# Kernel optimization log

Hardware: AMD Instinct MI355X
Metric: run time of the kernel (lower is better)

Reference implementation:

```python
import jax, jax.numpy as jnp
import numpy as np

POOL = 7          # pool_size (hardcoded 7x7 bins in source)
TOTAL_BINS = POOL * POOL  # 49
ALPHA = 32        # channels per position-sensitive group
NUM_ROIS = 8192
H = W = 20        # feature-map size; source hardcodes img_w=img_h=20 for normalization
CROP = 2          # bin_crop_size = 14 // 7


def setup_inputs() -> dict:
    key = jax.random.key(0)
    k1, k2, k3 = jax.random.split(key, 3)
    img = jax.random.normal(k1, (1, H, W, TOTAL_BINS * ALPHA), dtype=jnp.float32)
    xy = jax.random.uniform(k2, (1, NUM_ROIS, 2), minval=0.0, maxval=14.0, dtype=jnp.float32)
    wh = jax.random.uniform(k3, (1, NUM_ROIS, 2), minval=2.0, maxval=6.0, dtype=jnp.float32)
    rois = jnp.concatenate([xy, wh], axis=-1)  # (1, R, 4) as (x, y, w, h)
    return {"img": img, "rois": rois}


def _ps_roi_align(img, rois):
    R = rois.shape[1]
    x, y, w, h = rois[0, :, 0], rois[0, :, 1], rois[0, :, 2], rois[0, :, 3]
    step_y = h / POOL
    step_x = w / POOL

    # bin index b = bin_x * POOL + bin_y (outer loop bin_x, inner bin_y in source)
    bin_x = jnp.repeat(jnp.arange(POOL, dtype=jnp.float32), POOL)  # (49,)
    bin_y = jnp.tile(jnp.arange(POOL, dtype=jnp.float32), POOL)    # (49,)

    # normalized box coords [y1, x1, y2, x2] per (bin, roi)
    y1 = (y[None, :] + bin_y[:, None] * step_y[None, :]) / 20.0          # (49, R)
    x1 = (x[None, :] + bin_x[:, None] * step_x[None, :]) / 20.0
    y2 = (y[None, :] + (bin_y[:, None] + 1.0) * step_y[None, :]) / 20.0
    x2 = (x[None, :] + (bin_x[:, None] + 1.0) * step_x[None, :]) / 20.0

    # tf.image.crop_and_resize with crop size (2,2): sample points are exactly
    # the box corners in pixel space: y1*(H-1), y2*(H-1) (and same for x).
    ys = jnp.stack([y1, y2], axis=-1) * (H - 1)  # (49, R, 2)
    xs = jnp.stack([x1, x2], axis=-1) * (W - 1)  # (49, R, 2)

    valid_y = (ys >= 0) & (ys <= H - 1)  # (49, R, 2)
    valid_x = (xs >= 0) & (xs <= W - 1)

    fy = jnp.floor(ys)
    fx = jnp.floor(xs)
    wy = ys - fy  # bilinear lerp weights
    wx = xs - fx
    y0i = jnp.clip(fy.astype(jnp.int32), 0, H - 1)
    y1i = jnp.clip(y0i + 1, 0, H - 1)
    x0i = jnp.clip(fx.astype(jnp.int32), 0, W - 1)
    x1i = jnp.clip(x0i + 1, 0, W - 1)

    # split channels into 49 position-sensitive groups of ALPHA: (49, H, W, ALPHA)
    f = img[0].reshape(H, W, TOTAL_BINS, ALPHA).transpose(2, 0, 1, 3)

    bidx = jnp.arange(TOTAL_BINS)[:, None, None, None]  # (49,1,1,1)
    Y0 = y0i[:, :, :, None]  # (49, R, 2, 1)
    Y1 = y1i[:, :, :, None]
    X0 = x0i[:, :, None, :]  # (49, R, 1, 2)
    X1 = x1i[:, :, None, :]

    v00 = f[bidx, Y0, X0]  # (49, R, 2, 2, ALPHA)
    v01 = f[bidx, Y0, X1]
    v10 = f[bidx, Y1, X0]
    v11 = f[bidx, Y1, X1]

    WY = wy[:, :, :, None, None]  # (49, R, 2, 1, 1)
    WX = wx[:, :, None, :, None]  # (49, R, 1, 2, 1)
    val = (v00 * (1 - WY) * (1 - WX) + v01 * (1 - WY) * WX
           + v10 * WY * (1 - WX) + v11 * WY * WX)

    mask = (valid_y[:, :, :, None] & valid_x[:, :, None, :])[..., None]
    val = jnp.where(mask, val, 0.0)

    pooled = val.mean(axis=(2, 3))  # (49, R, ALPHA), mean over 2x2 crop
    # concat along bin axis then reshape: out[0, r, bin_x, bin_y, a]
    out = pooled.transpose(1, 0, 2).reshape(1, R, POOL, POOL, ALPHA)
    return out


def reference(img, rois):
    return _ps_roi_align(img, rois)
```

## Files before the change

### kernel.cpp

```cpp
#include <hip/hip_runtime.h>


#define CH 1568
#define IMG_W 20
#define CELLS 400
#define ROIS_PER_BLOCK 256
#define IMG_F (CELLS * 32)
#define PKOFF IMG_F
#define LDS_FLOATS (IMG_F + ROIS_PER_BLOCK * 8)

typedef float vf4 __attribute__((ext_vector_type(4)));

__device__ __forceinline__ void axis_weights(float s0, float s1,
                                             int& b, float& W0, float& W1, float& W2)
{
    const float f0 = floorf(s0), f1 = floorf(s1);
    const float w0 = s0 - f0,    w1 = s1 - f1;
    const float v0 = (s0 >= 0.f && s0 <= 19.f) ? 1.f : 0.f;
    const float v1 = (s1 >= 0.f && s1 <= 19.f) ? 1.f : 0.f;
    const int c00 = min(max((int)f0, 0), 19);
    const int c01 = min(c00 + 1, 19);
    const int c10 = min(max((int)f1, 0), 19);
    const int c11 = min(c10 + 1, 19);
    b = c00;
    W0 = v0 * (1.f - w0);
    W1 = 0.f; W2 = 0.f;
    float t = v0 * w0;
    if (c01 == b) W0 += t; else W1 += t;
    t = v1 * (1.f - w1);
    if (c10 == b) W0 += t; else W1 += t;
    t = v1 * w1;
    const int d = c11 - b;
    W0 += (d == 0) ? t : 0.f;
    W1 += (d == 1) ? t : 0.f;
    W2 += (d == 2) ? t : 0.f;
}

__global__ __launch_bounds__(1024, 8) void psroi_kernel(
    const float* __restrict__ img,
    const float* __restrict__ rois,
    float* __restrict__ out)
{
    __shared__ __align__(16) float lds[LDS_FLOATS];

    const unsigned t     = threadIdx.x;
    const unsigned bin   = blockIdx.x % 49u;
    const unsigned chunk = blockIdx.x / 49u;
    const unsigned p     = bin / 7u;
    const unsigned q     = bin - p * 7u;

    {
        const float* src = img + bin * 32u;
        for (unsigned idx = t; idx < CELLS * 8u; idx += 1024u) {
            const unsigned cell = idx >> 3;
            const unsigned sub  = idx & 7u;
            const vf4 v = *(const vf4*)(src + (size_t)cell * CH + sub * 4u);
            *(vf4*)(&lds[cell * 32u + sub * 4u]) = v;
        }
    }

    if (t < ROIS_PER_BLOCK) {
        const unsigned r = chunk * ROIS_PER_BLOCK + t;
        const vf4 roi = ((const vf4*)rois)[r];
        const float step_x = roi.z * (1.0f / 7.0f);
        const float step_y = roi.w * (1.0f / 7.0f);
        const float s = 19.0f / 20.0f;
        const float sx0 = (roi.x + (float)p * step_x) * s;
        const float sx1 = (roi.x + (float)(p + 1) * step_x) * s;
        const float sy0 = (roi.y + (float)q * step_y) * s;
        const float sy1 = (roi.y + (float)(q + 1) * step_y) * s;

        int bx, by;
        float WX0, WX1, WX2, WY0, WY1, WY2;
        axis_weights(sx0, sx1, bx, WX0, WX1, WX2);
        axis_weights(sy0, sy1, by, WY0, WY1, WY2);

        vf4 p0, p1;
        p0.x = __int_as_float(bx);
        p0.y = __int_as_float(by);
        p0.z = WX0; p0.w = WX1;
        p1.x = WX2;
        p1.y = WY0 * 0.25f; p1.z = WY1 * 0.25f; p1.w = WY2 * 0.25f;
        *(vf4*)(&lds[PKOFF + t * 8u])     = p0;
        *(vf4*)(&lds[PKOFF + t * 8u + 4]) = p1;
    }

    __syncthreads();

    const unsigned g  = t >> 3;
    const unsigned s  = t & 7u;
    const unsigned sb = s << 4;
    const char* ldsb = (const char*)lds;

#pragma unroll
    for (int pass = 0; pass < 2; ++pass) {
        const unsigned rl = g + (unsigned)pass * 128u;

        const float* pkp = &lds[PKOFF + rl * 8u];
        const vf4 p0 = *(const vf4*)pkp;
        const vf4 p1 = *(const vf4*)(pkp + 4);
        const int bx = __float_as_int(p0.x);
        const int by = __float_as_int(p0.y);
        const float WX[3] = { p0.z, p0.w, p1.x };
        const float WY[3] = { p1.y, p1.z, p1.w };

        const unsigned colb[3] = { (unsigned)bx * 128u + sb,
                                   (unsigned)min(bx + 1, 19) * 128u + sb,
                                   (unsigned)min(bx + 2, 19) * 128u + sb };
        const unsigned rowb[3] = { (unsigned)by * 2560u,
                                   (unsigned)min(by + 1, 19) * 2560u,
                                   (unsigned)min(by + 2, 19) * 2560u };

        vf4 acc = { 0.f, 0.f, 0.f, 0.f };
#pragma unroll
        for (int i = 0; i < 3; ++i) {
#pragma unroll
            for (int j = 0; j < 3; ++j) {
                const vf4 v = *(const vf4*)(ldsb + (rowb[i] + colb[j]));
                acc += (WY[i] * WX[j]) * v;
            }
        }

        const size_t ob = ((size_t)chunk * ROIS_PER_BLOCK + rl) * (49u * 32u)
                        + bin * 32u + s * 4u;
        __builtin_nontemporal_store(acc, (vf4*)(out + ob));
    }
}

extern "C" void kernel_launch(void* const* d_in, const int* in_sizes, int n_in,
                              void* d_out, int out_size, void* d_ws, size_t ws_size,
                              hipStream_t stream) {
    const float* img  = (const float*)d_in[0];
    const float* rois = (const float*)d_in[1];
    float* out = (float*)d_out;
    hipLaunchKernelGGL(psroi_kernel, dim3(1568), dim3(1024), 0, stream, img, rois, out);
}
```

Measured before the change: 80.35 us.

## Drop LDS staging and gather bilinear samples directly from global memory

After: 88.54 us. 10.2% more time.

```diff
diff --git a/kernel.cpp b/kernel.cpp
--- a/kernel.cpp
+++ b/kernel.cpp
@@ -1,13 +1,8 @@
 #include <hip/hip_runtime.h>
 
 
-#define CH 1568
-#define IMG_W 20
-#define CELLS 400
-#define ROIS_PER_BLOCK 256
-#define IMG_F (CELLS * 32)
-#define PKOFF IMG_F
-#define LDS_FLOATS (IMG_F + ROIS_PER_BLOCK * 8)
+#define CH    1568
+#define ROW_F (20 * CH)
 
 typedef float vf4 __attribute__((ext_vector_type(4)));
 
@@ -36,95 +31,57 @@
     W2 += (d == 2) ? t : 0.f;
 }
 
-__global__ __launch_bounds__(1024, 8) void psroi_kernel(
+__global__ __launch_bounds__(256, 6) void psroi_kernel(
     const float* __restrict__ img,
     const float* __restrict__ rois,
     float* __restrict__ out)
 {
-    __shared__ __align__(16) float lds[LDS_FLOATS];
-
     const unsigned t     = threadIdx.x;
-    const unsigned bin   = blockIdx.x % 49u;
-    const unsigned chunk = blockIdx.x / 49u;
+    const unsigned bin   = blockIdx.x >> 8;
+    const unsigned chunk = blockIdx.x & 255u;
     const unsigned p     = bin / 7u;
     const unsigned q     = bin - p * 7u;
 
-    {
-        const float* src = img + bin * 32u;
-        for (unsigned idx = t; idx < CELLS * 8u; idx += 1024u) {
-            const unsigned cell = idx >> 3;
-            const unsigned sub  = idx & 7u;
-            const vf4 v = *(const vf4*)(src + (size_t)cell * CH + sub * 4u);
-            *(vf4*)(&lds[cell * 32u + sub * 4u]) = v;
+    const unsigned g = t >> 3;
+    const unsigned s = t & 7u;
+    const unsigned r = chunk * 32u + g;
+
+    const vf4 roi = ((const vf4*)rois)[r];
+    const float step_x = roi.z * (1.0f / 7.0f);
+    const float step_y = roi.w * (1.0f / 7.0f);
+    const float sc  = 19.0f / 20.0f;
+    const float sx0 = (roi.x + (float)p * step_x) * sc;
+    const float sx1 = (roi.x + (float)(p + 1) * step_x) * sc;
+    const float sy0 = (roi.y + (float)q * step_y) * sc;
+    const float sy1 = (roi.y + (float)(q + 1) * step_y) * sc;
+
+    int bx, by;
+    float WX[3], WY[3];
+    axis_weights(sx0, sx1, bx, WX[0], WX[1], WX[2]);
+    axis_weights(sy0, sy1, by, WY[0], WY[1], WY[2]);
+    WY[0] *= 0.25f; WY[1] *= 0.25f; WY[2] *= 0.25f;
+
+    const unsigned colf[3] = { (unsigned)bx * (unsigned)CH,
+                               (unsigned)min(bx + 1, 19) * (unsigned)CH,
+                               (unsigned)min(bx + 2, 19) * (unsigned)CH };
+    const unsigned rowf[3] = { (unsigned)by * (unsigned)ROW_F,
+                               (unsigned)min(by + 1, 19) * (unsigned)ROW_F,
+                               (unsigned)min(by + 2, 19) * (unsigned)ROW_F };
+
+    const float* base = img + bin * 32u + s * 4u;
+
+    vf4 acc = { 0.f, 0.f, 0.f, 0.f };
+#pragma unroll
+    for (int i = 0; i < 3; ++i) {
+#pragma unroll
+        for (int j = 0; j < 3; ++j) {
+            const vf4 v = *(const vf4*)(base + rowf[i] + colf[j]);
+            acc += (WY[i] * WX[j]) * v;
         }
     }
 
-    if (t < ROIS_PER_BLOCK) {
-        const unsigned r = chunk * ROIS_PER_BLOCK + t;
-        const vf4 roi = ((const vf4*)rois)[r];
-        const float step_x = roi.z * (1.0f / 7.0f);
-        const float step_y = roi.w * (1.0f / 7.0f);
-        const float s = 19.0f / 20.0f;
-        const float sx0 = (roi.x + (float)p * step_x) * s;
-        const float sx1 = (roi.x + (float)(p + 1) * step_x) * s;
-        const float sy0 = (roi.y + (float)q * step_y) * s;
-        const float sy1 = (roi.y + (float)(q + 1) * step_y) * s;
-
-        int bx, by;
-        float WX0, WX1, WX2, WY0, WY1, WY2;
-        axis_weights(sx0, sx1, bx, WX0, WX1, WX2);
-        axis_weights(sy0, sy1, by, WY0, WY1, WY2);
-
-        vf4 p0, p1;
-        p0.x = __int_as_float(bx);
-        p0.y = __int_as_float(by);
-        p0.z = WX0; p0.w = WX1;
-        p1.x = WX2;
-        p1.y = WY0 * 0.25f; p1.z = WY1 * 0.25f; p1.w = WY2 * 0.25f;
-        *(vf4*)(&lds[PKOFF + t * 8u])     = p0;
-        *(vf4*)(&lds[PKOFF + t * 8u + 4]) = p1;
-    }
-
-    __syncthreads();
-
-    const unsigned g  = t >> 3;
-    const unsigned s  = t & 7u;
-    const unsigned sb = s << 4;
-    const char* ldsb = (const char*)lds;
-
-#pragma unroll
-    for (int pass = 0; pass < 2; ++pass) {
-        const unsigned rl = g + (unsigned)pass * 128u;
-
-        const float* pkp = &lds[PKOFF + rl * 8u];
-        const vf4 p0 = *(const vf4*)pkp;
-        const vf4 p1 = *(const vf4*)(pkp + 4);
-        const int bx = __float_as_int(p0.x);
-        const int by = __float_as_int(p0.y);
-        const float WX[3] = { p0.z, p0.w, p1.x };
-        const float WY[3] = { p1.y, p1.z, p1.w };
-
-        const unsigned colb[3] = { (unsigned)bx * 128u + sb,
-                                   (unsigned)min(bx + 1, 19) * 128u + sb,
-                                   (unsigned)min(bx + 2, 19) * 128u + sb };
-        const unsigned rowb[3] = { (unsigned)by * 2560u,
-                                   (unsigned)min(by + 1, 19) * 2560u,
-                                   (unsigned)min(by + 2, 19) * 2560u };
-
-        vf4 acc = { 0.f, 0.f, 0.f, 0.f };
-#pragma unroll
-        for (int i = 0; i < 3; ++i) {
-#pragma unroll
-            for (int j = 0; j < 3; ++j) {
-                const vf4 v = *(const vf4*)(ldsb + (rowb[i] + colb[j]));
-                acc += (WY[i] * WX[j]) * v;
-            }
-        }
-
-        const size_t ob = ((size_t)chunk * ROIS_PER_BLOCK + rl) * (49u * 32u)
-                        + bin * 32u + s * 4u;
-        __builtin_nontemporal_store(acc, (vf4*)(out + ob));
-    }
+    const size_t ob = (size_t)r * 1568u + bin * 32u + s * 4u;
+    __builtin_nontemporal_store(acc, (vf4*)(out + ob));
 }
 
 extern "C" void kernel_launch(void* const* d_in, const int* in_sizes, int n_in,
@@ -133,5 +90,5 @@
     const float* img  = (const float*)d_in[0];
     const float* rois = (const float*)d_in[1];
     float* out = (float*)d_out;
-    hipLaunchKernelGGL(psroi_kernel, dim3(1568), dim3(1024), 0, stream, img, rois, out);
+    hipLaunchKernelGGL(psroi_kernel, dim3(49 * 256), dim3(256), 0, stream, img, rois, out);
 }
```
